# Kernel optimization log

Measured on AMD Instinct MI355X. Metric: run time of the kernel, lower is better.

The kernel has to match this reference:

```python
import jax, jax.numpy as jnp
import numpy as np

N, L, S, C, H = 4, 2048, 4096, 256, 8
D = C // H          # head dim = 32
HID = 4 * C         # mlp hidden = 1024
LN_EPS = 1e-5
LA_EPS = 1e-6


def _layer_norm(x, g, b):
    m = x.mean(-1, keepdims=True)
    v = ((x - m) ** 2).mean(-1, keepdims=True)
    return (x - m) * jax.lax.rsqrt(v + LN_EPS) * g + b


def _linear_attention(q, k, v):
    # q: [N,L,H,D], k/v: [N,S,H,D]  (elu feature map linear attention)
    Q = jax.nn.elu(q) + 1.0
    K = jax.nn.elu(k) + 1.0
    v_len = v.shape[1]
    KV = jnp.einsum('nshd,nshv->nhdv', K, v / v_len)
    Z = 1.0 / (jnp.einsum('nlhd,nhd->nlh', Q, K.sum(axis=1)) + LA_EPS)
    return jnp.einsum('nlhd,nhdv,nlh->nlhv', Q, KV, Z) * v_len


def setup_inputs() -> dict:
    key = jax.random.key(0)
    ks = jax.random.split(key, 32)
    f32 = jnp.float32
    w = lambda k, *s: (jax.random.normal(k, s, dtype=f32) * 0.02)
    inp = {
        'tgt': jax.random.normal(ks[0], (N, L, C), dtype=f32),
        'memory': jax.random.normal(ks[1], (N, S, C), dtype=f32),
        'tgt_pos': jax.random.normal(ks[2], (N, L, C), dtype=f32),
        'pos_embed': w(ks[3], 1, S, C),
        # layer norms
        'ln1_g': jnp.ones((C,), f32), 'ln1_b': jnp.zeros((C,), f32),
        'ln2_g': jnp.ones((C,), f32), 'ln2_b': jnp.zeros((C,), f32),
        'ln3_g': jnp.ones((C,), f32), 'ln3_b': jnp.zeros((C,), f32),
        # self-attn projections (stored (in,out))
        'wq': w(ks[4], C, C), 'bq': jnp.zeros((C,), f32),
        'wk': w(ks[5], C, C), 'bk': jnp.zeros((C,), f32),
        'wv': w(ks[6], C, C), 'bv': jnp.zeros((C,), f32),
        'w_merge': w(ks[7], C, C),
        # cross-attn (CCAttention) projections
        'cwq': w(ks[8], C, C), 'cbq': jnp.zeros((C,), f32),
        'cwk': w(ks[9], C, C), 'cbk': jnp.zeros((C,), f32),
        'cwv': w(ks[10], C, C), 'cbv': jnp.zeros((C,), f32),
        'cwo': w(ks[11], C, C), 'cbo': jnp.zeros((C,), f32),
        # mlp (fc1 -> dwconv3x3 -> gelu -> fc2)
        'mw1': w(ks[12], C, HID), 'mb1': jnp.zeros((HID,), f32),
        'dw_k': w(ks[13], HID, 1, 3, 3), 'dw_b': jnp.zeros((HID,), f32),
        'mw2': w(ks[14], HID, C), 'mb2': jnp.zeros((C,), f32),
        'num_points': L,
    }
    return inp


def reference(tgt, memory, tgt_pos, pos_embed,
              ln1_g, ln1_b, ln2_g, ln2_b, ln3_g, ln3_b,
              wq, bq, wk, bk, wv, bv, w_merge,
              cwq, cbq, cwk, cbk, cwv, cbv, cwo, cbo,
              mw1, mb1, dw_k, dw_b, mw2, mb2, num_points):
    n, l, c = tgt.shape
    # ---- self attention (linear attention) ----
    tgt2 = _layer_norm(tgt, ln1_g, ln1_b)
    qk = tgt2 + tgt_pos
    q = (qk @ wq + bq).reshape(n, l, H, D)
    k = (qk @ wk + bk).reshape(n, l, H, D)
    v = (tgt2 @ wv + bv).reshape(n, l, H, D)
    msg = _linear_attention(q, k, v).reshape(n, l, c) @ w_merge
    tgt = tgt + msg  # dropout is identity in eval
    # ---- cross attention (CCAttention, softmax MHA) ----
    tgt2 = _layer_norm(tgt, ln2_g, ln2_b)
    mem = memory + pos_embed
    cq = (tgt2 @ cwq + cbq).reshape(n, l, H, D)
    ck = (mem @ cwk + cbk).reshape(n, -1, H, D)
    cv = (mem @ cwv + cbv).reshape(n, -1, H, D)
    scale = D ** -0.5
    attn = jax.nn.softmax(jnp.einsum('nlhd,nshd->nhls', cq, ck) * scale, axis=-1)
    cmsg = jnp.einsum('nhls,nshd->nlhd', attn, cv).reshape(n, l, c) @ cwo + cbo
    tgt = tgt + cmsg
    # ---- MLP with depthwise conv over (num_points, 1) grid ----
    x = _layer_norm(tgt, ln3_g, ln3_b)
    h = x @ mw1 + mb1                                   # [n,l,HID]
    hi = h.transpose(0, 2, 1).reshape(n, HID, num_points, 1)
    hi = jax.lax.conv_general_dilated(
        hi, dw_k, window_strides=(1, 1), padding=((1, 1), (1, 1)),
        feature_group_count=HID,
        dimension_numbers=('NCHW', 'OIHW', 'NCHW'))
    hi = hi + dw_b[None, :, None, None]
    h = hi.reshape(n, HID, l).transpose(0, 2, 1)
    h = jax.nn.gelu(h, approximate=False)
    mlp_out = h @ mw2 + mb2
    return tgt + mlp_out
```

## Files before the change

kernel.cpp:

```cpp
#include <hip/hip_runtime.h>
#include <hip/hip_bf16.h>
#include <math.h>

#define NB 4
#define LL 2048
#define SS 4096
#define CC 256
#define HH 8
#define DD 32
#define HIDN 1024
#define NSPLIT 2

using bf16 = __hip_bfloat16;
typedef __attribute__((ext_vector_type(8))) short short8;
typedef __attribute__((ext_vector_type(4))) short short4v;
typedef __attribute__((ext_vector_type(4))) float floatx4;

__device__ __forceinline__ float b2f(bf16 x) { return __bfloat162float(x); }
__device__ __forceinline__ short f2bs(float x) {
    bf16 h = __float2bfloat16(x);
    return *(short*)&h;
}
__device__ __forceinline__ short f2bs_fast(float x) {
    return (short)(__float_as_uint(x) >> 16);
}
__device__ __forceinline__ float s2f(short s) {
    bf16 h = *(bf16*)&s;
    return __bfloat162float(h);
}

#if __has_builtin(__builtin_amdgcn_exp2f)
#define EXP2(x) __builtin_amdgcn_exp2f(x)
#else
#define EXP2(x) exp2f(x)
#endif

__device__ __forceinline__ bool probe_f32(const unsigned* p) {
    return p[0] == 0x3F800000u;
}
__device__ __forceinline__ float ldx(const void* p, size_t i, bool f32m) {
    return f32m ? ((const float*)p)[i] : b2f(((const bf16*)p)[i]);
}

__global__ __launch_bounds__(256)
void zero_kernel(float* __restrict__ p, int n) {
    int i = blockIdx.x * 256 + threadIdx.x;
    if (i < n) p[i] = 0.0f;
}

struct WPack { const void* p[10]; };

__global__ __launch_bounds__(256)
void wprep_kernel(WPack pk, short* __restrict__ dst,
                  const unsigned* __restrict__ probe) {
    const bool f32m = probe_f32(probe);
    const int z = blockIdx.z;
    const int K = (z == 9) ? 1024 : 256;
    const int N = (z == 8) ? 1024 : 256;
    const size_t off = (z < 8) ? (size_t)z * 65536 : (z == 8 ? 524288u : 786432u);
    const int k0 = blockIdx.y * 64, n0 = blockIdx.x * 64;
    if (k0 >= K || n0 >= N) return;
    __shared__ float T[64][65];
    const void* src = pk.p[z];
    const int tid = threadIdx.x;
    #pragma unroll
    for (int p = 0; p < 16; ++p) {
        int idx = tid + p * 256;
        int r = idx >> 6, c = idx & 63;
        T[r][c] = ldx(src, (size_t)(k0 + r) * N + n0 + c, f32m);
    }
    __syncthreads();
    short* d = dst + off;
    #pragma unroll
    for (int p = 0; p < 16; ++p) {
        int idx = tid + p * 256;
        int c2 = idx >> 6, r2 = idx & 63;
        d[(size_t)(n0 + c2) * K + k0 + r2] = f2bs(T[r2][c2]);
    }
}

__global__ __launch_bounds__(256)
void ln_kernel(const void* __restrict__ xr, const float* __restrict__ xf,
               const void* __restrict__ g, const void* __restrict__ bta,
               const void* __restrict__ pos,
               short* __restrict__ y, short* __restrict__ y2,
               const unsigned* __restrict__ probe) {
    const bool f32m = probe_f32(probe);
    const int row = blockIdx.x;
    const int c = threadIdx.x;
    const size_t base = (size_t)row * CC;
    float x = xr ? ldx(xr, base + c, f32m) : xf[base + c];
    float a = x, b = x * x;
    #pragma unroll
    for (int off = 32; off; off >>= 1) {
        a += __shfl_down(a, off);
        b += __shfl_down(b, off);
    }
    __shared__ float sa[4], sb[4];
    if ((c & 63) == 0) { sa[c >> 6] = a; sb[c >> 6] = b; }
    __syncthreads();
    float s1 = sa[0] + sa[1] + sa[2] + sa[3];
    float s2 = sb[0] + sb[1] + sb[2] + sb[3];
    float mean = s1 * (1.0f / CC);
    float var = s2 * (1.0f / CC) - mean * mean;
    float inv = rsqrtf(var + 1e-5f);
    float yv = (x - mean) * inv * ldx(g, c, f32m) + ldx(bta, c, f32m);
    y[base + c] = f2bs(yv);
    if (y2) y2[base + c] = f2bs(yv + ldx(pos, base + c, f32m));
}

__global__ __launch_bounds__(256)
void addpos_kernel(const void* __restrict__ mem, const void* __restrict__ pos,
                   short* __restrict__ out, const unsigned* __restrict__ probe) {
    const bool f32m = probe_f32(probe);
    const int row = blockIdx.x;
    const int c = threadIdx.x;
    const int s = row & (SS - 1);
    out[(size_t)row * CC + c] =
        f2bs(ldx(mem, (size_t)row * CC + c, f32m) + ldx(pos, (size_t)s * CC + c, f32m));
}

template <int BM, int BN, int EPI, int OUTMODE, int TRANSC2>
__global__ __launch_bounds__(256)
void gemm_mfma_kernel(const short* __restrict__ A, const short* __restrict__ Bt,
                      const void* __restrict__ bias, const void* __restrict__ bias2,
                      const float* __restrict__ residF, const void* __restrict__ residR,
                      void* __restrict__ Cout, void* __restrict__ Cout2,
                      int M, int N, int K, const unsigned* __restrict__ probe) {
    const bool f32m = probe_f32(probe);
    constexpr int WM = BM / 2, AI = WM / 16;
    constexpr int WN = BN / 2, BJ = WN / 16;
    constexpr int ACH = (BM == 128) ? 4 : 2;
    constexpr int BCH = (BN == 128) ? 4 : 2;
    __shared__ __attribute__((aligned(16))) short As[BM][72];
    __shared__ __attribute__((aligned(16))) short Bs[BN][72];
    const int tid = threadIdx.x;
    const int ln = tid & 15, quad = (tid >> 4) & 3, w = tid >> 6;
    const int wm = (w & 1) * WM, wn = (w >> 1) * WN;
    const int bm = blockIdx.y * BM, bn = blockIdx.x * BN;
    const int ar = (BM == 128) ? (tid >> 1) : (tid >> 2);
    const int ac = (BM == 128) ? ((tid & 1) * 32) : ((tid & 3) * 16);
    const int br = (BN == 128) ? (tid >> 1) : (tid >> 2);
    const int bc = (BN == 128) ? ((tid & 1) * 32) : ((tid & 3) * 16);

    short8 pa[ACH], pb[BCH];
    {
        const short* ag = &A[(size_t)(bm + ar) * K + ac];
        #pragma unroll
        for (int t = 0; t < ACH; ++t) pa[t] = *(const short8*)(ag + t * 8);
        const short* bg = &Bt[(size_t)(bn + br) * K + bc];
        #pragma unroll
        for (int t = 0; t < BCH; ++t) pb[t] = *(const short8*)(bg + t * 8);
    }
    floatx4 acc[AI][BJ] = {};
    for (int k0 = 0; k0 < K; k0 += 64) {
        #pragma unroll
        for (int t = 0; t < ACH; ++t) *(short8*)&As[ar][ac + t * 8] = pa[t];
        #pragma unroll
        for (int t = 0; t < BCH; ++t) *(short8*)&Bs[br][bc + t * 8] = pb[t];
        if (k0 + 64 < K) {
            const short* ag = &A[(size_t)(bm + ar) * K + k0 + 64 + ac];
            #pragma unroll
            for (int t = 0; t < ACH; ++t) pa[t] = *(const short8*)(ag + t * 8);
            const short* bg = &Bt[(size_t)(bn + br) * K + k0 + 64 + bc];
            #pragma unroll
            for (int t = 0; t < BCH; ++t) pb[t] = *(const short8*)(bg + t * 8);
        }
        __syncthreads();
        #pragma unroll
        for (int ks = 0; ks < 2; ++ks) {
            short8 af[AI], bf[BJ];
            #pragma unroll
            for (int i = 0; i < AI; ++i)
                af[i] = *(const short8*)&As[wm + i * 16 + ln][ks * 32 + quad * 8];
            #pragma unroll
            for (int j = 0; j < BJ; ++j)
                bf[j] = *(const short8*)&Bs[wn + j * 16 + ln][ks * 32 + quad * 8];
            #pragma unroll
            for (int i = 0; i < AI; ++i)
                #pragma unroll
                for (int j = 0; j < BJ; ++j)
                    acc[i][j] = __builtin_amdgcn_mfma_f32_16x16x32_bf16(af[i], bf[j], acc[i][j], 0, 0, 0);
        }
        __syncthreads();
    }
    #pragma unroll
    for (int i = 0; i < AI; ++i)
        #pragma unroll
        for (int j = 0; j < BJ; ++j) {
            const int gr0 = bm + wm + i * 16 + quad * 4;
            const int gc = bn + wn + j * 16 + ln;
            const bool hi = (Cout2 != nullptr) && (gc >= 256);
            const int col = hi ? gc - 256 : gc;
            const int sN = Cout2 ? 256 : N;
            void* co = hi ? Cout2 : Cout;
            const void* bb = hi ? bias2 : bias;
            float vv[4];
            #pragma unroll
            for (int r = 0; r < 4; ++r) {
                float v = acc[i][j][r];
                if (bb) v += ldx(bb, col, f32m);
                if (EPI == 1) v = (v > 0.0f) ? (v + 1.0f) : __expf(v);
                const size_t o = (size_t)(gr0 + r) * sN + col;
                if (residF) v += residF[o];
                if (residR) v += ldx(residR, o, f32m);
                vv[r] = v;
            }
            if (TRANSC2 && hi) {
                const int nb = gr0 >> 12;
                const int s = gr0 & (SS - 1);
                short4v pk4 = {f2bs(vv[0]), f2bs(vv[1]), f2bs(vv[2]), f2bs(vv[3])};
                *(short4v*)&((short*)co)[((size_t)nb * CC + col) * SS + s] = pk4;
            } else {
                #pragma unroll
                for (int r = 0; r < 4; ++r) {
                    const size_t o = (size_t)(gr0 + r) * sN + col;
                    if (OUTMODE == 0) ((float*)co)[o] = vv[r];
                    else if (OUTMODE == 2) ((short*)co)[o] = f2bs(vv[r]);
                    else {
                        if (f32m) ((float*)co)[o] = vv[r];
                        else      ((bf16*)co)[o] = __float2bfloat16(vv[r]);
                    }
                }
            }
        }
}

#define KVSPLIT 16
__global__ __launch_bounds__(256)
void linattn_kv_kernel(const float* __restrict__ Kp, const float* __restrict__ Vp,
                       float* __restrict__ KV, float* __restrict__ Ksum) {
    const int h = blockIdx.x, n = blockIdx.y, z = blockIdx.z;
    __shared__ __attribute__((aligned(16))) float Kt[64][33];
    __shared__ __attribute__((aligned(16))) float Vt[64][32];
    const int tid = threadIdx.x;
    const int d = tid >> 3, e0 = (tid & 7) * 4;
    const int sbeg = z * (LL / KVSPLIT), send = sbeg + (LL / KVSPLIT);
    float acc[4] = {}, ks = 0.0f;
    for (int s0 = sbeg; s0 < send; s0 += 64) {
        #pragma unroll
        for (int p = 0; p < 8; ++p) {
            int idx = tid + p * 256;
            int r = idx >> 5, c = idx & 31;
            size_t gaddr = (size_t)((n * LL) + s0 + r) * CC + h * DD + c;
            Kt[r][c] = Kp[gaddr];
            Vt[r][c] = Vp[gaddr];
        }
        __syncthreads();
        for (int s = 0; s < 64; ++s) {
            float kd = Kt[s][d];
            ks += kd;
            float4 v4 = *(const float4*)&Vt[s][e0];
            acc[0] += kd * v4.x; acc[1] += kd * v4.y;
            acc[2] += kd * v4.z; acc[3] += kd * v4.w;
        }
        __syncthreads();
    }
    float* kvp = &KV[(size_t)((n * HH + h) * DD + d) * DD + e0];
    atomicAdd(&kvp[0], acc[0]); atomicAdd(&kvp[1], acc[1]);
    atomicAdd(&kvp[2], acc[2]); atomicAdd(&kvp[3], acc[3]);
    if ((tid & 7) == 0) atomicAdd(&Ksum[(n * HH + h) * DD + d], ks);
}

__global__ __launch_bounds__(256)
void linattn_out_kernel(const float* __restrict__ Qp, const float* __restrict__ KV,
                        const float* __restrict__ Ksum, short* __restrict__ Out) {
    const int lt = blockIdx.x, h = blockIdx.y, n = blockIdx.z;
    __shared__ float KVs[32][33];
    __shared__ float Ks[32];
    __shared__ float Qs[64][33];
    const int tid = threadIdx.x;
    for (int p = 0; p < 4; ++p) {
        int idx = tid + p * 256;
        KVs[idx >> 5][idx & 31] = KV[(size_t)(n * HH + h) * (DD * DD) + idx];
    }
    if (tid < 32) Ks[tid] = Ksum[(n * HH + h) * DD + tid];
    for (int p = 0; p < 8; ++p) {
        int idx = tid + p * 256;
        int r = idx >> 5, c = idx & 31;
        Qs[r][c] = Qp[(size_t)((n * LL) + lt * 64 + r) * CC + h * DD + c];
    }
    __syncthreads();
    const int e = tid & 31;
    for (int ii = 0; ii < 8; ++ii) {
        const int i = (tid >> 5) + ii * 8;
        float num = 0.0f, den = 0.0f;
        for (int d = 0; d < 32; ++d) {
            float q = Qs[i][d];
            num += q * KVs[d][e];
            den += q * Ks[d];
        }
        Out[(size_t)((n * LL) + lt * 64 + i) * CC + h * DD + e] = f2bs(num / (den + 1e-6f));
    }
}

__global__ __launch_bounds__(256)
void flash_mfma_kernel(const short* __restrict__ Q, const short* __restrict__ K,
                       const short* __restrict__ V,
                       float* __restrict__ Of, float* __restrict__ Lp) {
    const int lt = blockIdx.x, h = blockIdx.y;
    const int n = blockIdx.z >> 1, sp = blockIdx.z & 1;
    const int tid = threadIdx.x;
    const int ln = tid & 15;
    const int quad = (tid >> 4) & 3;
    const int w = tid >> 6;
    const int NT = NB * LL;
    const float qscale = 0.17677669529663687f * 1.4426950408889634f;

    __shared__ __attribute__((aligned(16))) short Qs[64][40];
    __shared__ __attribute__((aligned(16))) short Ks[64][40];
    __shared__ __attribute__((aligned(16))) short Vp[32][72];

    {
        const int r = tid >> 2, c0 = (tid & 3) * 8;
        short8 qv = *(const short8*)&Q[(size_t)((n * LL) + lt * 64 + r) * CC + h * DD + c0];
        short tmp[8];
        #pragma unroll
        for (int j = 0; j < 8; ++j) tmp[j] = f2bs(s2f(qv[j]) * qscale);
        *(short8*)&Qs[r][c0] = *(short8*)tmp;
    }
    __syncthreads();

    short8 bQ = *(const short8*)&Qs[w * 16 + ln][quad * 8];

    const short one_b = (short)0x3F80;
    const short8 ones8 = {one_b, one_b, one_b, one_b, one_b, one_b, one_b, one_b};

    floatx4 o0 = {0.f, 0.f, 0.f, 0.f};
    floatx4 o1 = {0.f, 0.f, 0.f, 0.f};
    floatx4 o2 = {0.f, 0.f, 0.f, 0.f};
    const floatx4 zinit = {-24.f, -24.f, -24.f, -24.f};

    const int r_st = tid >> 2, c0_st = (tid & 3) * 8;
    const int e_st = tid >> 3, m_st = tid & 7;
    const int K32 = (m_st >> 2) * 32;
    const int h4 = ((m_st >> 1) & 1) * 4;
    const int q0s = (2 * m_st) & 3;
    const int slotA = K32 + q0s * 8 + h4;
    const int slotB = K32 + (q0s + 1) * 8 + h4;

    const int sbeg = sp * (SS / NSPLIT), send = sbeg + (SS / NSPLIT);
    for (int s0 = sbeg; s0 < send; s0 += 64) {
        *(short8*)&Ks[r_st][c0_st] =
            *(const short8*)&K[(size_t)((n * SS) + s0 + r_st) * CC + h * DD + c0_st];
        {
            short8 vv = *(const short8*)&V[((size_t)n * CC + h * DD + e_st) * SS + s0 + m_st * 8];
            short4v lo = {vv[0], vv[1], vv[2], vv[3]};
            short4v hi = {vv[4], vv[5], vv[6], vv[7]};
            *(short4v*)&Vp[e_st][slotA] = lo;
            *(short4v*)&Vp[e_st][slotB] = hi;
        }
        __syncthreads();

        floatx4 sc[4];
        #pragma unroll
        for (int g = 0; g < 4; ++g) {
            short8 aK = *(const short8*)&Ks[g * 16 + ln][quad * 8];
            sc[g] = __builtin_amdgcn_mfma_f32_16x16x32_bf16(aK, bQ, zinit, 0, 0, 0);
        }

        #pragma unroll
        for (int ks = 0; ks < 2; ++ks) {
            union { unsigned u[4]; short8 s8; } cvt;
            #pragma unroll
            for (int jj = 0; jj < 4; ++jj) {
                const int j0 = 2 * jj, j1 = 2 * jj + 1;
                float p0 = EXP2(sc[2 * ks + (j0 >> 2)][j0 & 3]);
                float p1 = EXP2(sc[2 * ks + (j1 >> 2)][j1 & 3]);
                cvt.u[jj] = __builtin_amdgcn_perm(
                    __float_as_uint(p1), __float_as_uint(p0), 0x07060302u);
            }
            short8 aP = cvt.s8;
            short8 bV0 = *(const short8*)&Vp[ln][ks * 32 + quad * 8];
            short8 bV1 = *(const short8*)&Vp[16 + ln][ks * 32 + quad * 8];
            o0 = __builtin_amdgcn_mfma_f32_16x16x32_bf16(aP, bV0, o0, 0, 0, 0);
            o1 = __builtin_amdgcn_mfma_f32_16x16x32_bf16(aP, bV1, o1, 0, 0, 0);
            o2 = __builtin_amdgcn_mfma_f32_16x16x32_bf16(aP, ones8, o2, 0, 0, 0);
        }
        __syncthreads();
    }

    const int rowbase = lt * 64 + w * 16;
    if (ln == 0) {
        #pragma unroll
        for (int r = 0; r < 4; ++r)
            Lp[((size_t)sp * NT + (size_t)n * LL + rowbase + quad * 4 + r) * HH + h] = o2[r];
    }
    #pragma unroll
    for (int r = 0; r < 4; ++r) {
        const size_t row = (size_t)n * LL + rowbase + quad * 4 + r;
        float* o = &Of[((size_t)sp * NT + row) * CC + h * DD];
        o[ln] = o0[r];
        o[16 + ln] = o1[r];
    }
}

__global__ __launch_bounds__(256)
void flash_merge_kernel(const float* __restrict__ Of, const float* __restrict__ Lp,
                        short* __restrict__ O) {
    const int row = blockIdx.x, c = threadIdx.x, h = c >> 5;
    const size_t NT = (size_t)NB * LL;
    float l = Lp[(size_t)row * HH + h] + Lp[(NT + row) * HH + h];
    float v = Of[(size_t)row * CC + c] + Of[NT * CC + (size_t)row * CC + c];
    O[(size_t)row * CC + c] = f2bs(v / l);
}

__global__ __launch_bounds__(256)
void dwconv_gelu_kernel(const short* __restrict__ H1, const void* __restrict__ wk,
                        const void* __restrict__ wb, short* __restrict__ H2,
                        const unsigned* __restrict__ probe) {
    const bool f32m = probe_f32(probe);
    const int row = blockIdx.x;
    const int l = row & (LL - 1);
    const int c0 = threadIdx.x * 4;
    const short* cur = &H1[(size_t)row * HIDN + c0];
    short4v xc = *(const short4v*)cur;
    short4v xm = {}, xp = {};
    if (l > 0)      xm = *(const short4v*)(cur - HIDN);
    if (l < LL - 1) xp = *(const short4v*)(cur + HIDN);
    short r[4];
    #pragma unroll
    for (int j = 0; j < 4; ++j) {
        int ch = c0 + j;
        float wm = ldx(wk, ch * 9 + 1, f32m);
        float w0 = ldx(wk, ch * 9 + 4, f32m);
        float wp = ldx(wk, ch * 9 + 7, f32m);
        float v = s2f(xm[j]) * wm + s2f(xc[j]) * w0 + s2f(xp[j]) * wp + ldx(wb, ch, f32m);
        r[j] = f2bs(0.5f * v * (1.0f + erff(v * 0.70710678118654752f)));
    }
    short4v out = {r[0], r[1], r[2], r[3]};
    *(short4v*)&H2[(size_t)row * HIDN + c0] = out;
}

extern "C" void kernel_launch(void* const* d_in, const int* in_sizes, int n_in,
                              void* d_out, int out_size, void* d_ws, size_t ws_size,
                              hipStream_t stream) {
    const void* tgt      = d_in[0];
    const void* memory   = d_in[1];
    const void* tgt_pos  = d_in[2];
    const void* pos_emb  = d_in[3];
    const void* ln1_g = d_in[4],  *ln1_b = d_in[5];
    const void* ln2_g = d_in[6],  *ln2_b = d_in[7];
    const void* ln3_g = d_in[8],  *ln3_b = d_in[9];
    const void* wq = d_in[10], *bq = d_in[11];
    const void* wk = d_in[12], *bk = d_in[13];
    const void* wv = d_in[14], *bv = d_in[15];
    const void* w_merge = d_in[16];
    const void* cwq = d_in[17], *cbq = d_in[18];
    const void* cwk = d_in[19], *cbk = d_in[20];
    const void* cwv = d_in[21], *cbv = d_in[22];
    const void* cwo = d_in[23], *cbo = d_in[24];
    const void* mw1 = d_in[25], *mb1 = d_in[26];
    const void* dw_k = d_in[27], *dw_b = d_in[28];
    const void* mw2 = d_in[29], *mb2 = d_in[30];
    const unsigned* probe = (const unsigned*)d_in[4];

    char* w = (char*)d_ws;
    const size_t MB = 1024 * 1024;
    short* lnout_b = (short*)(w + 0 * MB);
    short* qk_b    = (short*)(w + 4 * MB);
    float* Tbuf    = (float*)(w + 8 * MB);
    float* phiq    = (float*)(w + 16 * MB);
    float* phik    = (float*)(w + 24 * MB);
    float* vbuf    = (float*)(w + 32 * MB);
    float* KVb     = (float*)(w + 40 * MB);
    float* Ksb     = (float*)(w + 40 * MB + 131072);
    short* cqbuf   = (short*)(w + 41 * MB);
    short* membuf  = (short*)(w + 45 * MB);
    short* ckbuf   = (short*)(w + 53 * MB);
    short* cvT     = (short*)(w + 69 * MB);
    short* flashO  = (short*)(w + 77 * MB);
    short* wT      = (short*)(w + 81 * MB);
    float* Ofb     = (float*)(w + 16 * MB);
    float* Lpb     = (float*)(w + 32 * MB);
    short* H1      = (short*)(w + 16 * MB);
    short* H2      = (short*)(w + 32 * MB);

    short* wqT  = wT + 0 * 65536;
    short* wvT  = wT + 2 * 65536;
    short* wmT  = wT + 3 * 65536;
    short* cwqT = wT + 4 * 65536;
    short* cwkT = wT + 5 * 65536;
    short* cwoT = wT + 7 * 65536;
    short* mw1T = wT + 524288;
    short* mw2T = wT + 786432;

    const int NT = NB * LL;
    const int NS = NB * SS;
    const dim3 blk(256);

    WPack pk;
    pk.p[0] = wq;  pk.p[1] = wk;  pk.p[2] = wv;  pk.p[3] = w_merge;
    pk.p[4] = cwq; pk.p[5] = cwk; pk.p[6] = cwv; pk.p[7] = cwo;
    pk.p[8] = mw1; pk.p[9] = mw2;
    wprep_kernel<<<dim3(16, 16, 10), blk, 0, stream>>>(pk, wT, probe);
    zero_kernel<<<dim3(137), blk, 0, stream>>>(KVb, 35072);

    ln_kernel<<<NT, blk, 0, stream>>>(tgt, nullptr, ln1_g, ln1_b, tgt_pos, lnout_b, qk_b, probe);
    gemm_mfma_kernel<64, 64, 1, 0, 0><<<dim3(8, NT / 64), blk, 0, stream>>>(
        qk_b, wqT, bq, bk, nullptr, nullptr, phiq, phik, NT, 512, CC, probe);
    gemm_mfma_kernel<64, 64, 0, 0, 0><<<dim3(4, NT / 64), blk, 0, stream>>>(
        lnout_b, wvT, bv, nullptr, nullptr, nullptr, vbuf, nullptr, NT, CC, CC, probe);
    linattn_kv_kernel<<<dim3(HH, NB, KVSPLIT), blk, 0, stream>>>(phik, vbuf, KVb, Ksb);
    linattn_out_kernel<<<dim3(LL / 64, HH, NB), blk, 0, stream>>>(phiq, KVb, Ksb, (short*)vbuf);
    gemm_mfma_kernel<64, 64, 0, 0, 0><<<dim3(4, NT / 64), blk, 0, stream>>>(
        (short*)vbuf, wmT, nullptr, nullptr, nullptr, tgt, Tbuf, nullptr, NT, CC, CC, probe);

    ln_kernel<<<NT, blk, 0, stream>>>(nullptr, Tbuf, ln2_g, ln2_b, nullptr, lnout_b, nullptr, probe);
    addpos_kernel<<<NS, blk, 0, stream>>>(memory, pos_emb, membuf, probe);
    gemm_mfma_kernel<64, 64, 0, 2, 0><<<dim3(4, NT / 64), blk, 0, stream>>>(
        lnout_b, cwqT, cbq, nullptr, nullptr, nullptr, cqbuf, nullptr, NT, CC, CC, probe);
    gemm_mfma_kernel<64, 64, 0, 2, 1><<<dim3(8, NS / 64), blk, 0, stream>>>(
        membuf, cwkT, cbk, cbv, nullptr, nullptr, ckbuf, cvT, NS, 512, CC, probe);
    flash_mfma_kernel<<<dim3(LL / 64, HH, NB * NSPLIT), blk, 0, stream>>>(
        cqbuf, ckbuf, cvT, Ofb, Lpb);
    flash_merge_kernel<<<NT, blk, 0, stream>>>(Ofb, Lpb, flashO);
    gemm_mfma_kernel<64, 64, 0, 0, 0><<<dim3(4, NT / 64), blk, 0, stream>>>(
        flashO, cwoT, cbo, nullptr, Tbuf, nullptr, Tbuf, nullptr, NT, CC, CC, probe);

    ln_kernel<<<NT, blk, 0, stream>>>(nullptr, Tbuf, ln3_g, ln3_b, nullptr, lnout_b, nullptr, probe);
    gemm_mfma_kernel<64, 64, 0, 2, 0><<<dim3(16, NT / 64), blk, 0, stream>>>(
        lnout_b, mw1T, mb1, nullptr, nullptr, nullptr, H1, nullptr, NT, HIDN, CC, probe);
    dwconv_gelu_kernel<<<NT, blk, 0, stream>>>(H1, dw_k, dw_b, H2, probe);
    gemm_mfma_kernel<64, 64, 0, 1, 0><<<dim3(4, NT / 64), blk, 0, stream>>>(
        H2, mw2T, mb2, nullptr, Tbuf, nullptr, d_out, nullptr, NT, CC, HIDN, probe);

    (void)in_sizes; (void)n_in; (void)out_size; (void)ws_size;
}
```

Baseline: 428.7 us.

## Double-buffer K/V tiles with register prefetch in flash attention kernel

The cross-attention flash kernel now preloads the next K and V tiles into registers while the current tile is being consumed. It alternates between two shared-memory buffers, which drops the trailing barrier so there is one __syncthreads per iteration instead of two. The aim is to hide global load latency behind the MFMA and exp work. In exchange it doubles the K/V shared memory and raises register pressure. It also relies on the single barrier being enough to separate writes to a buffer from reads of it two iterations earlier.

Result: no change. 428.7 us (-0.0%).

```diff
diff --git a/kernel.cpp b/kernel.cpp
--- a/kernel.cpp
+++ b/kernel.cpp
@@ -308,8 +308,8 @@
     const float qscale = 0.17677669529663687f * 1.4426950408889634f;
 
     __shared__ __attribute__((aligned(16))) short Qs[64][40];
-    __shared__ __attribute__((aligned(16))) short Ks[64][40];
-    __shared__ __attribute__((aligned(16))) short Vp[32][72];
+    __shared__ __attribute__((aligned(16))) short Ks[2][64][40];
+    __shared__ __attribute__((aligned(16))) short Vp[2][32][72];
 
     {
         const int r = tid >> 2, c0 = (tid & 3) * 8;
@@ -339,23 +339,33 @@
     const int slotA = K32 + q0s * 8 + h4;
     const int slotB = K32 + (q0s + 1) * 8 + h4;
 
-    const int sbeg = sp * (SS / NSPLIT), send = sbeg + (SS / NSPLIT);
-    for (int s0 = sbeg; s0 < send; s0 += 64) {
-        *(short8*)&Ks[r_st][c0_st] =
-            *(const short8*)&K[(size_t)((n * SS) + s0 + r_st) * CC + h * DD + c0_st];
+    const int sbeg = sp * (SS / NSPLIT);
+    constexpr int NIT = (SS / NSPLIT) / 64;
+
+    const short* kptr = &K[(size_t)((n * SS) + sbeg + r_st) * CC + h * DD + c0_st];
+    const short* vptr = &V[((size_t)n * CC + h * DD + e_st) * SS + sbeg + m_st * 8];
+    short8 kreg = *(const short8*)kptr;
+    short8 vreg = *(const short8*)vptr;
+
+    for (int it = 0; it < NIT; ++it) {
+        const int buf = it & 1;
+        *(short8*)&Ks[buf][r_st][c0_st] = kreg;
         {
-            short8 vv = *(const short8*)&V[((size_t)n * CC + h * DD + e_st) * SS + s0 + m_st * 8];
-            short4v lo = {vv[0], vv[1], vv[2], vv[3]};
-            short4v hi = {vv[4], vv[5], vv[6], vv[7]};
-            *(short4v*)&Vp[e_st][slotA] = lo;
-            *(short4v*)&Vp[e_st][slotB] = hi;
+            short4v lo = {vreg[0], vreg[1], vreg[2], vreg[3]};
+            short4v hi = {vreg[4], vreg[5], vreg[6], vreg[7]};
+            *(short4v*)&Vp[buf][e_st][slotA] = lo;
+            *(short4v*)&Vp[buf][e_st][slotB] = hi;
+        }
+        if (it + 1 < NIT) {
+            kreg = *(const short8*)(kptr + (size_t)(it + 1) * 64 * CC);
+            vreg = *(const short8*)(vptr + (it + 1) * 64);
         }
         __syncthreads();
 
         floatx4 sc[4];
         #pragma unroll
         for (int g = 0; g < 4; ++g) {
-            short8 aK = *(const short8*)&Ks[g * 16 + ln][quad * 8];
+            short8 aK = *(const short8*)&Ks[buf][g * 16 + ln][quad * 8];
             sc[g] = __builtin_amdgcn_mfma_f32_16x16x32_bf16(aK, bQ, zinit, 0, 0, 0);
         }
 
@@ -371,13 +381,12 @@
                     __float_as_uint(p1), __float_as_uint(p0), 0x07060302u);
             }
             short8 aP = cvt.s8;
-            short8 bV0 = *(const short8*)&Vp[ln][ks * 32 + quad * 8];
-            short8 bV1 = *(const short8*)&Vp[16 + ln][ks * 32 + quad * 8];
+            short8 bV0 = *(const short8*)&Vp[buf][ln][ks * 32 + quad * 8];
+            short8 bV1 = *(const short8*)&Vp[buf][16 + ln][ks * 32 + quad * 8];
             o0 = __builtin_amdgcn_mfma_f32_16x16x32_bf16(aP, bV0, o0, 0, 0, 0);
             o1 = __builtin_amdgcn_mfma_f32_16x16x32_bf16(aP, bV1, o1, 0, 0, 0);
             o2 = __builtin_amdgcn_mfma_f32_16x16x32_bf16(aP, ones8, o2, 0, 0, 0);
         }
-        __syncthreads();
     }
 
     const int rowbase = lt * 64 + w * 16;
```
